# Kernel optimization log

Measured on AMD Instinct MI355X. Metric: run time of the kernel, lower is better.

## Reference

```python
import jax, jax.numpy as jnp
import numpy as np

N_NODES = 16384   # dim_size (number of aggregation groups)
DEG = 16          # neighbors per node
H = 128           # hidden_dim
E = N_NODES * DEG # total neighbor rows


def setup_inputs() -> dict:
    key = jax.random.key(0)
    k1, k2, k3 = jax.random.split(key, 3)
    x = jax.random.normal(k1, (E, H), dtype=jnp.float32)
    # sorted segment ids, DEG neighbors per node (ragged in general; uniform here)
    index = jnp.repeat(jnp.arange(N_NODES, dtype=jnp.int32), DEG)
    # torch LSTM params: gates stacked [i, f, g, o] -> [4H, H]
    W_ih = jax.random.normal(k2, (4 * H, H), dtype=jnp.float32) * 0.02  # xavier gain=0.02 scale
    W_hh = jax.random.normal(k3, (4 * H, H), dtype=jnp.float32) * (1.0 / np.sqrt(H))
    b_ih = jnp.zeros((4 * H,), jnp.float32)
    b_hh = jnp.zeros((4 * H,), jnp.float32)
    return {"x": x, "index": index, "W_ih": W_ih, "W_hh": W_hh,
            "b_ih": b_ih, "b_hh": b_hh, "dim_size": N_NODES}


def reference(x, index, W_ih, W_hh, b_ih, b_hh, dim_size):
    # Faithful to LSTMAggregator.forward: per-group gather of neighbor rows,
    # single-layer LSTM over each group's sequence, final hidden state h_n
    # written to out[group]; empty groups stay zero. (The original's randperm
    # shuffle is nondeterministic and omitted: neighbors kept in index order.)
    x = jnp.nan_to_num(x, nan=0.0)
    E_, Hd = x.shape

    # --- pack ragged groups into a padded [N, L, H] tensor ---
    order = jnp.argsort(index, stable=True)
    idx_s = index[order]
    counts = jax.ops.segment_sum(jnp.ones((E_,), jnp.int32), idx_s, num_segments=dim_size)
    starts = jnp.cumsum(counts) - counts           # exclusive prefix sum
    pos = jnp.arange(E_, dtype=jnp.int32) - starts[idx_s]  # position within group
    L = int(jnp.max(counts))                       # static at call time (concrete inputs)

    x_s = x[order]
    padded = jnp.zeros((dim_size, L, Hd), x.dtype).at[idx_s, pos].set(x_s)  # [N, L, H]
    valid = jnp.arange(L)[None, :] < counts[:, None]                        # [N, L]

    # --- batched masked LSTM scan over time ---
    bias = b_ih + b_hh
    h0 = jnp.zeros((dim_size, Hd), x.dtype)

    def step(carry, inp):
        h, c = carry
        xt, m = inp                                 # xt: [N, H], m: [N]
        gates = xt @ W_ih.T + h @ W_hh.T + bias     # [N, 4H], gate order i,f,g,o
        i, f, g, o = jnp.split(gates, 4, axis=-1)
        i = jax.nn.sigmoid(i); f = jax.nn.sigmoid(f)
        g = jnp.tanh(g);       o = jax.nn.sigmoid(o)
        c_new = f * c + i * g
        h_new = o * jnp.tanh(c_new)
        m = m[:, None]
        return (jnp.where(m, h_new, h), jnp.where(m, c_new, c)), None

    xs = (jnp.swapaxes(padded, 0, 1), valid.T)      # time-major [L, N, H], [L, N]
    (h_final, _), _ = jax.lax.scan(step, (h0, h0), xs)
    return jnp.nan_to_num(h_final, nan=0.0)        # [dim_size, H]
```

## Files before the change

### kernel.cpp

```cpp
#include <hip/hip_runtime.h>

#define DEG      16
#define HDIM     128
#define MB       32
#define NTHREADS 512

typedef __attribute__((ext_vector_type(8))) short  short8;
typedef __attribute__((ext_vector_type(4))) float  floatx4;

__device__ __forceinline__ unsigned short f2bf(float f) {
  union { float f; unsigned int u; } v; v.f = f;
  unsigned int u = v.u;
  u += 0x7fffu + ((u >> 16) & 1u);
  return (unsigned short)(u >> 16);
}

__device__ __forceinline__ float fsig(float x) {
  return __builtin_amdgcn_rcpf(1.0f + __expf(-x));
}
__device__ __forceinline__ float ftanh(float x) {
  return 1.0f - 2.0f * __builtin_amdgcn_rcpf(1.0f + __expf(2.0f * x));
}

__global__ void convert_w_kernel(const float* __restrict__ Wih,
                                 const float* __restrict__ Whh,
                                 unsigned short* __restrict__ Wsw) {
  int i    = blockIdx.x * 256 + threadIdx.x;
  int lane = i & 63;
  int frag = i >> 6;
  int kt = frag >> 5;
  int wg = frag & 31;
  int w  = wg >> 2;
  int g  = wg & 3;
  int j  = g * 128 + w * 16 + (lane & 15);
  int k0 = kt * 32 + (lane >> 4) * 8;
  const float* src = (k0 < HDIM) ? (Wih + (size_t)j * HDIM + k0)
                                 : (Whh + (size_t)j * HDIM + (k0 - HDIM));
  short8 o;
  #pragma unroll
  for (int e = 0; e < 8; ++e) o[e] = (short)f2bf(src[e]);
  *(short8*)(Wsw + (size_t)i * 8) = o;
}

__global__ __launch_bounds__(NTHREADS, 2)
void lstm_agg_kernel(const float* __restrict__ x,
                     const float* __restrict__ b_ih,
                     const float* __restrict__ b_hh,
                     const unsigned short* __restrict__ Wsw,
                     float* __restrict__ out) {
  __shared__ __align__(16) unsigned short As[2][MB * 256];

  const int tid  = threadIdx.x;
  const int w_id = tid >> 6;
  const int lane = tid & 63;
  const int l15  = lane & 15;
  const int q    = lane >> 4;
  const int node0 = blockIdx.x * MB;

  const int j_g = w_id * 16 + l15;

  float bias[4];
  #pragma unroll
  for (int g = 0; g < 4; ++g) bias[g] = b_ih[g * 128 + j_g] + b_hh[g * 128 + j_g];

  short8 breg[2][4];
  #pragma unroll
  for (int kt = 0; kt < 2; ++kt)
    #pragma unroll
    for (int g = 0; g < 4; ++g) {
      int fi = kt * 32 + w_id * 4 + g;
      breg[kt][g] = *(const short8*)(Wsw + ((size_t)fi * 64 + lane) * 8);
    }

  floatx4 c[2], h[2];
  #pragma unroll
  for (int mt = 0; mt < 2; ++mt) {
    floatx4 z = {0.0f, 0.0f, 0.0f, 0.0f};
    c[mt] = z; h[mt] = z;
  }

  const int m_x = tid >> 4;
  const int kc  = tid & 15;
  const float* xbase = x + ((size_t)(node0 + m_x) * DEG) * HDIM + kc * 8;
  const int xch = (kc ^ (m_x & 7)) * 8;
  const int hchunk = (HDIM + j_g) >> 3;
  const int hkl = j_g & 7;

  floatx4 xp0 = ((const floatx4*)xbase)[0];
  floatx4 xp1 = ((const floatx4*)xbase)[1];

  {
    short8 p;
    #pragma unroll
    for (int e = 0; e < 4; ++e) { p[e] = (short)f2bf(xp0[e]); p[e + 4] = (short)f2bf(xp1[e]); }
    *(short8*)&As[0][m_x * 256 + xch] = p;
    unsigned short hz = f2bf(0.0f);
    #pragma unroll
    for (int mt = 0; mt < 2; ++mt)
      #pragma unroll
      for (int r = 0; r < 4; ++r) {
        int m = mt * 16 + q * 4 + r;
        As[0][m * 256 + ((hchunk ^ (m & 7)) << 3) + hkl] = hz;
      }
  }
  xp0 = ((const floatx4*)(xbase + HDIM))[0];
  xp1 = ((const floatx4*)(xbase + HDIM))[1];

  #pragma unroll 1
  for (int t = 0; t < DEG; ++t) {
    __syncthreads();
    const int buf = t & 1;

    const unsigned short* Wp = Wsw;
    asm volatile("" : "+s"(Wp));

    floatx4 acc[4][2];
    #pragma unroll
    for (int g = 0; g < 4; ++g) {
      floatx4 bv = {bias[g], bias[g], bias[g], bias[g]};
      #pragma unroll
      for (int mt = 0; mt < 2; ++mt) acc[g][mt] = bv;
    }

    #pragma unroll
    for (int kt = 0; kt < 8; ++kt) {
      short8 af[2];
      #pragma unroll
      for (int mt = 0; mt < 2; ++mt) {
        int m = mt * 16 + l15;
        int chunk = (kt * 4 + q) ^ (m & 7);
        af[mt] = *(const short8*)&As[buf][m * 256 + chunk * 8];
      }
      short8 bfr[4];
      if (kt < 2) {
        #pragma unroll
        for (int g = 0; g < 4; ++g) bfr[g] = breg[kt][g];
      } else {
        #pragma unroll
        for (int g = 0; g < 4; ++g) {
          int fi = kt * 32 + w_id * 4 + g;
          bfr[g] = *(const short8*)(Wp + ((size_t)fi * 64 + lane) * 8);
        }
      }
      #pragma unroll
      for (int g = 0; g < 4; ++g)
        #pragma unroll
        for (int mt = 0; mt < 2; ++mt)
          acc[g][mt] = __builtin_amdgcn_mfma_f32_16x16x32_bf16(af[mt], bfr[g], acc[g][mt], 0, 0, 0);
    }

    #pragma unroll
    for (int mt = 0; mt < 2; ++mt)
      #pragma unroll
      for (int r = 0; r < 4; ++r) {
        float iv = fsig (acc[0][mt][r]);
        float fv = fsig (acc[1][mt][r]);
        float gv = ftanh(acc[2][mt][r]);
        float ov = fsig (acc[3][mt][r]);
        float cn = fv * c[mt][r] + iv * gv;
        c[mt][r] = cn;
        float hv = ov * ftanh(cn);
        h[mt][r] = hv;
        if (t + 1 < DEG) {
          int m = mt * 16 + q * 4 + r;
          As[buf ^ 1][m * 256 + ((hchunk ^ (m & 7)) << 3) + hkl] = f2bf(hv);
        }
      }

    if (t + 1 < DEG) {
      short8 p;
      #pragma unroll
      for (int e = 0; e < 4; ++e) { p[e] = (short)f2bf(xp0[e]); p[e + 4] = (short)f2bf(xp1[e]); }
      *(short8*)&As[buf ^ 1][m_x * 256 + xch] = p;
      if (t + 2 < DEG) {
        const float* xb = xbase + (size_t)(t + 2) * HDIM;
        xp0 = ((const floatx4*)xb)[0];
        xp1 = ((const floatx4*)xb)[1];
      }
    }
  }

  #pragma unroll
  for (int mt = 0; mt < 2; ++mt)
    #pragma unroll
    for (int r = 0; r < 4; ++r) {
      int m = mt * 16 + q * 4 + r;
      out[(size_t)(node0 + m) * HDIM + j_g] = h[mt][r];
    }
}

extern "C" void kernel_launch(void* const* d_in, const int* in_sizes, int n_in,
                              void* d_out, int out_size, void* d_ws, size_t ws_size,
                              hipStream_t stream) {
  const float* x   = (const float*)d_in[0];
  const float* Wih = (const float*)d_in[2];
  const float* Whh = (const float*)d_in[3];
  const float* bih = (const float*)d_in[4];
  const float* bhh = (const float*)d_in[5];
  unsigned short* Wsw = (unsigned short*)d_ws;
  float* out = (float*)d_out;

  hipLaunchKernelGGL(convert_w_kernel, dim3(64), dim3(256), 0, stream, Wih, Whh, Wsw);

  int nodes   = in_sizes[0] / (DEG * HDIM);
  int nblocks = nodes / MB;
  hipLaunchKernelGGL(lstm_agg_kernel, dim3(nblocks), dim3(NTHREADS), 0, stream,
                     x, bih, bhh, Wsw, out);
}
```

Before: 280.8 us.

## Software-pipeline input projection ahead of recurrence; split X/H LDS and stage weights

The LSTM step now computes the input projection x_{t+1}·W_ih one step early, interleaved with the activation of step t, so each step's critical path only carries the h·W_hh MFMAs. X and H get separate double-buffered LDS arrays with a new swizzle. Part of W_ih is staged in LDS while the rest stays in registers or global memory. bf16 packing now uses v_cvt_pk_bf16_f32, and the time loop is unrolled by two with ping-pong accumulators. The cost is more accumulator registers and about 32KB of extra LDS, which may reduce occupancy below the 2-block launch bound.

Result: faster. 262.0 us (-6.7%).

```diff
diff --git a/kernel.cpp b/kernel.cpp
--- a/kernel.cpp
+++ b/kernel.cpp
@@ -7,12 +7,21 @@
 
 typedef __attribute__((ext_vector_type(8))) short  short8;
 typedef __attribute__((ext_vector_type(4))) float  floatx4;
+typedef __attribute__((ext_vector_type(4))) unsigned int uintx4;
+
+#define MFMA(A,B,C) __builtin_amdgcn_mfma_f32_16x16x32_bf16(A,B,C,0,0,0)
 
 __device__ __forceinline__ unsigned short f2bf(float f) {
   union { float f; unsigned int u; } v; v.f = f;
   unsigned int u = v.u;
   u += 0x7fffu + ((u >> 16) & 1u);
   return (unsigned short)(u >> 16);
+}
+
+__device__ __forceinline__ unsigned int cvtpk(float lo, float hi) {
+  unsigned int r;
+  asm("v_cvt_pk_bf16_f32 %0, %1, %2" : "=v"(r) : "v"(lo), "v"(hi));
+  return r;
 }
 
 __device__ __forceinline__ float fsig(float x) {
@@ -42,13 +51,100 @@
   *(short8*)(Wsw + (size_t)i * 8) = o;
 }
 
+#define ACT_X(MT, PAR, ACCP, ACCQ, LAST_, CS)                                  \
+  {                                                                            \
+    float hv[4];                                                               \
+    _Pragma("unroll")                                                          \
+    for (int r = 0; r < 4; ++r) {                                              \
+      float iv = fsig (ACCP[0][MT][r]);                                        \
+      float fv = fsig (ACCP[1][MT][r]);                                        \
+      float gv = ftanh(ACCP[2][MT][r]);                                        \
+      float ov = fsig (ACCP[3][MT][r]);                                        \
+      float cn = fv * CS[r] + iv * gv;                                         \
+      CS[r] = cn;                                                              \
+      hv[r] = ov * ftanh(cn);                                                  \
+    }                                                                          \
+    if (LAST_) {                                                               \
+      float* ob = out + (size_t)(node0 + MT * 16 + q * 4) * HDIM + j_g;        \
+      _Pragma("unroll")                                                        \
+      for (int r = 0; r < 4; ++r) ob[r * HDIM] = hv[r];                        \
+    } else {                                                                   \
+      unsigned int p01 = cvtpk(hv[0], hv[1]);                                  \
+      unsigned int p23 = cvtpk(hv[2], hv[3]);                                  \
+      *(unsigned short*)(hwp[0] + ((PAR ^ 1) * 8192 + MT * 4096)) = (unsigned short)p01;         \
+      *(unsigned short*)(hwp[1] + ((PAR ^ 1) * 8192 + MT * 4096)) = (unsigned short)(p01 >> 16); \
+      *(unsigned short*)(hwp[2] + ((PAR ^ 1) * 8192 + MT * 4096)) = (unsigned short)p23;         \
+      *(unsigned short*)(hwp[3] + ((PAR ^ 1) * 8192 + MT * 4096)) = (unsigned short)(p23 >> 16); \
+            \
+      short8 ax0 = *(const short8*)(xsE + (PAR ^ 1) * 8192 + MT * 4096 + 0);   \
+      short8 ax1 = *(const short8*)(xsO + (PAR ^ 1) * 8192 + MT * 4096 + 64);  \
+      short8 ax2 = *(const short8*)(xsE + (PAR ^ 1) * 8192 + MT * 4096 + 128); \
+      short8 ax3 = *(const short8*)(xsO + (PAR ^ 1) * 8192 + MT * 4096 + 192); \
+      short8 w2[4];                                                            \
+      _Pragma("unroll")                                                        \
+      for (int g = 0; g < 4; ++g) w2[g] = *(const short8*)(wlB + g * 1024);    \
+      _Pragma("unroll")                                                        \
+      for (int g = 0; g < 4; ++g) {                                            \
+        floatx4 bv = {bias[g], bias[g], bias[g], bias[g]};                     \
+        floatx4 t0 = MFMA(ax0, breg[0][g], bv);                                \
+        t0 = MFMA(ax1, breg[1][g], t0);                                        \
+        t0 = MFMA(ax2, w2[g], t0);                                             \
+        ACCQ[g][MT] = MFMA(ax3, b3[g], t0);                                    \
+      }                                                                        \
+    }                                                                          \
+  }
+
+#define STEP(T, PAR, ACCP, ACCQ, WITH_H, LAST_)                                \
+  {                                                                            \
+    const unsigned short* Wp = Wsw;                                            \
+    asm volatile("" : "+s"(Wp));                     \
+    if (WITH_H) {                                                              \
+      _Pragma("unroll")                                                        \
+      for (int kh = 0; kh < 4; ++kh) {                                         \
+        const unsigned short* Wk = Wp + ((size_t)((4 + kh) * 32 + w_id * 4) * 64 + lane) * 8; \
+        short8 bfr[4];                                                         \
+        _Pragma("unroll")                                                      \
+        for (int g = 0; g < 4; ++g) bfr[g] = *(const short8*)(Wk + g * 512);   \
+        const char* hb = (kh & 1) ? hsO : hsE;                                 \
+        short8 ah0 = *(const short8*)(hb + PAR * 8192 + 0    + kh * 64);       \
+        short8 ah1 = *(const short8*)(hb + PAR * 8192 + 4096 + kh * 64);       \
+        _Pragma("unroll")                                                      \
+        for (int g = 0; g < 4; ++g) {                                          \
+          ACCP[g][0] = MFMA(ah0, bfr[g], ACCP[g][0]);                          \
+          ACCP[g][1] = MFMA(ah1, bfr[g], ACCP[g][1]);                          \
+        }                                                                      \
+      }                                                                        \
+    }                                                                          \
+    short8 b3[4];                                                              \
+    if (!LAST_) {                                                              \
+      const unsigned short* W3 = Wp + ((size_t)(96 + w_id * 4) * 64 + lane) * 8; \
+      _Pragma("unroll")                                                        \
+      for (int g = 0; g < 4; ++g) b3[g] = *(const short8*)(W3 + g * 512);      \
+    }                                                                          \
+    ACT_X(0, PAR, ACCP, ACCQ, LAST_, cs0)                                      \
+    ACT_X(1, PAR, ACCP, ACCQ, LAST_, cs1)                                      \
+    if (!LAST_ && (T) + 2 < DEG) {                                             \
+      uintx4 p;                                                                \
+      p[0] = cvtpk(xp0[0], xp0[1]); p[1] = cvtpk(xp0[2], xp0[3]);              \
+      p[2] = cvtpk(xp1[0], xp1[1]); p[3] = cvtpk(xp1[2], xp1[3]);              \
+      *(uintx4*)(xsW + PAR * 8192) = p;                                        \
+      if ((T) + 3 < DEG) {                                                     \
+        const float* xq_ = xb0 + (size_t)((T) + 3) * HDIM;                     \
+        xp0 = ((const floatx4*)xq_)[0]; xp1 = ((const floatx4*)xq_)[1];        \
+      }                                                                        \
+    }                                                                          \
+    __syncthreads();                                                           \
+  }
+
 __global__ __launch_bounds__(NTHREADS, 2)
 void lstm_agg_kernel(const float* __restrict__ x,
                      const float* __restrict__ b_ih,
                      const float* __restrict__ b_hh,
                      const unsigned short* __restrict__ Wsw,
                      float* __restrict__ out) {
-  __shared__ __align__(16) unsigned short As[2][MB * 256];
+  __shared__ __align__(16) unsigned short Xs[2 * MB * HDIM];
+  __shared__ __align__(16) unsigned short Hs[2 * MB * HDIM];
+  __shared__ __align__(16) unsigned short Wl[32 * 512];
 
   const int tid  = threadIdx.x;
   const int w_id = tid >> 6;
@@ -56,7 +152,6 @@
   const int l15  = lane & 15;
   const int q    = lane >> 4;
   const int node0 = blockIdx.x * MB;
-
   const int j_g = w_id * 16 + l15;
 
   float bias[4];
@@ -72,121 +167,91 @@
       breg[kt][g] = *(const short8*)(Wsw + ((size_t)fi * 64 + lane) * 8);
     }
 
-  floatx4 c[2], h[2];
-  #pragma unroll
-  for (int mt = 0; mt < 2; ++mt) {
-    floatx4 z = {0.0f, 0.0f, 0.0f, 0.0f};
-    c[mt] = z; h[mt] = z;
+  #pragma unroll
+  for (int i = 0; i < 4; ++i) {
+    int o = tid * 32 + i * 8;
+    *(short8*)&Wl[o] = *(const short8*)(Wsw + 2 * 32 * 512 + o);
+  }
+
+  const int fA  = (l15 & 7) ^ ((l15 & 8) >> 2);
+  const int qx  = (q ^ (fA & 3)) << 4;
+  const int f64 = (fA >> 2) << 6;
+  const char* xsE = (const char*)Xs + l15 * 256 + qx + f64;
+  const char* xsO = (const char*)Xs + l15 * 256 + qx - f64;
+  const char* hsE = (const char*)Hs + l15 * 256 + qx + f64;
+  const char* hsO = (const char*)Hs + l15 * 256 + qx - f64;
+
+  const char* wlB = (const char*)Wl + w_id * 4096 + lane * 16;
+
+  const int hc  = j_g >> 3;
+  const int hkl = j_g & 7;
+  char* hwp[4];
+  #pragma unroll
+  for (int r = 0; r < 4; ++r) {
+    int m  = q * 4 + r;
+    int fr = (m & 7) ^ ((m & 8) >> 2);
+    hwp[r] = (char*)Hs + m * 256 + ((hc ^ fr) << 4) + hkl * 2;
   }
 
   const int m_x = tid >> 4;
   const int kc  = tid & 15;
-  const float* xbase = x + ((size_t)(node0 + m_x) * DEG) * HDIM + kc * 8;
-  const int xch = (kc ^ (m_x & 7)) * 8;
-  const int hchunk = (HDIM + j_g) >> 3;
-  const int hkl = j_g & 7;
-
-  floatx4 xp0 = ((const floatx4*)xbase)[0];
-  floatx4 xp1 = ((const floatx4*)xbase)[1];
+  const int fX  = (m_x & 7) ^ ((m_x & 8) >> 2);
+  const float* xb0 = x + ((size_t)(node0 + m_x) * DEG) * HDIM + kc * 8;
+  char* xsW = (char*)Xs + m_x * 256 + ((kc ^ fX) << 4);
+
+  floatx4 cs0 = {0.f, 0.f, 0.f, 0.f};
+  floatx4 cs1 = {0.f, 0.f, 0.f, 0.f};
+  floatx4 accA[4][2], accB[4][2];
+  floatx4 xp0, xp1;
 
   {
-    short8 p;
+    floatx4 u0 = ((const floatx4*)xb0)[0], u1 = ((const floatx4*)xb0)[1];
+    uintx4 p;
+    p[0] = cvtpk(u0[0], u0[1]); p[1] = cvtpk(u0[2], u0[3]);
+    p[2] = cvtpk(u1[0], u1[1]); p[3] = cvtpk(u1[2], u1[3]);
+    *(uintx4*)xsW = p;
+    u0 = ((const floatx4*)(xb0 + HDIM))[0]; u1 = ((const floatx4*)(xb0 + HDIM))[1];
+    p[0] = cvtpk(u0[0], u0[1]); p[1] = cvtpk(u0[2], u0[3]);
+    p[2] = cvtpk(u1[0], u1[1]); p[3] = cvtpk(u1[2], u1[3]);
+    *(uintx4*)(xsW + 8192) = p;
+    xp0 = ((const floatx4*)(xb0 + 2 * HDIM))[0];
+    xp1 = ((const floatx4*)(xb0 + 2 * HDIM))[1];
+  }
+  __syncthreads();
+
+  {
+    short8 b3p[4];
+    const unsigned short* W3 = Wsw + ((size_t)(96 + w_id * 4) * 64 + lane) * 8;
     #pragma unroll
-    for (int e = 0; e < 4; ++e) { p[e] = (short)f2bf(xp0[e]); p[e + 4] = (short)f2bf(xp1[e]); }
-    *(short8*)&As[0][m_x * 256 + xch] = p;
-    unsigned short hz = f2bf(0.0f);
+    for (int g = 0; g < 4; ++g) b3p[g] = *(const short8*)(W3 + g * 512);
     #pragma unroll
-    for (int mt = 0; mt < 2; ++mt)
+    for (int mt = 0; mt < 2; ++mt) {
+      short8 ax0 = *(const short8*)(xsE + mt * 4096 + 0);
+      short8 ax1 = *(const short8*)(xsO + mt * 4096 + 64);
+      short8 ax2 = *(const short8*)(xsE + mt * 4096 + 128);
+      short8 ax3 = *(const short8*)(xsO + mt * 4096 + 192);
+      short8 w2[4];
       #pragma unroll
-      for (int r = 0; r < 4; ++r) {
-        int m = mt * 16 + q * 4 + r;
-        As[0][m * 256 + ((hchunk ^ (m & 7)) << 3) + hkl] = hz;
-      }
-  }
-  xp0 = ((const floatx4*)(xbase + HDIM))[0];
-  xp1 = ((const floatx4*)(xbase + HDIM))[1];
-
-  #pragma unroll 1
-  for (int t = 0; t < DEG; ++t) {
-    __syncthreads();
-    const int buf = t & 1;
-
-    const unsigned short* Wp = Wsw;
-    asm volatile("" : "+s"(Wp));
-
-    floatx4 acc[4][2];
-    #pragma unroll
-    for (int g = 0; g < 4; ++g) {
-      floatx4 bv = {bias[g], bias[g], bias[g], bias[g]};
+      for (int g = 0; g < 4; ++g) w2[g] = *(const short8*)(wlB + g * 1024);
       #pragma unroll
-      for (int mt = 0; mt < 2; ++mt) acc[g][mt] = bv;
-    }
-
-    #pragma unroll
-    for (int kt = 0; kt < 8; ++kt) {
-      short8 af[2];
-      #pragma unroll
-      for (int mt = 0; mt < 2; ++mt) {
-        int m = mt * 16 + l15;
-        int chunk = (kt * 4 + q) ^ (m & 7);
-        af[mt] = *(const short8*)&As[buf][m * 256 + chunk * 8];
-      }
-      short8 bfr[4];
-      if (kt < 2) {
-        #pragma unroll
-        for (int g = 0; g < 4; ++g) bfr[g] = breg[kt][g];
-      } else {
-        #pragma unroll
-        for (int g = 0; g < 4; ++g) {
-          int fi = kt * 32 + w_id * 4 + g;
-          bfr[g] = *(const short8*)(Wp + ((size_t)fi * 64 + lane) * 8);
-        }
-      }
-      #pragma unroll
-      for (int g = 0; g < 4; ++g)
-        #pragma unroll
-        for (int mt = 0; mt < 2; ++mt)
-          acc[g][mt] = __builtin_amdgcn_mfma_f32_16x16x32_bf16(af[mt], bfr[g], acc[g][mt], 0, 0, 0);
-    }
-
-    #pragma unroll
-    for (int mt = 0; mt < 2; ++mt)
-      #pragma unroll
-      for (int r = 0; r < 4; ++r) {
-        float iv = fsig (acc[0][mt][r]);
-        float fv = fsig (acc[1][mt][r]);
-        float gv = ftanh(acc[2][mt][r]);
-        float ov = fsig (acc[3][mt][r]);
-        float cn = fv * c[mt][r] + iv * gv;
-        c[mt][r] = cn;
-        float hv = ov * ftanh(cn);
-        h[mt][r] = hv;
-        if (t + 1 < DEG) {
-          int m = mt * 16 + q * 4 + r;
-          As[buf ^ 1][m * 256 + ((hchunk ^ (m & 7)) << 3) + hkl] = f2bf(hv);
-        }
-      }
-
-    if (t + 1 < DEG) {
-      short8 p;
-      #pragma unroll
-      for (int e = 0; e < 4; ++e) { p[e] = (short)f2bf(xp0[e]); p[e + 4] = (short)f2bf(xp1[e]); }
-      *(short8*)&As[buf ^ 1][m_x * 256 + xch] = p;
-      if (t + 2 < DEG) {
-        const float* xb = xbase + (size_t)(t + 2) * HDIM;
-        xp0 = ((const floatx4*)xb)[0];
-        xp1 = ((const floatx4*)xb)[1];
+      for (int g = 0; g < 4; ++g) {
+        floatx4 bv = {bias[g], bias[g], bias[g], bias[g]};
+        floatx4 t0 = MFMA(ax0, breg[0][g], bv);
+        t0 = MFMA(ax1, breg[1][g], t0);
+        t0 = MFMA(ax2, w2[g], t0);
+        accA[g][mt] = MFMA(ax3, b3p[g], t0);
       }
     }
   }
-
-  #pragma unroll
-  for (int mt = 0; mt < 2; ++mt)
-    #pragma unroll
-    for (int r = 0; r < 4; ++r) {
-      int m = mt * 16 + q * 4 + r;
-      out[(size_t)(node0 + m) * HDIM + j_g] = h[mt][r];
-    }
+  __syncthreads();
+
+  STEP(0, 0, accA, accB, 0, 0)
+  #pragma unroll 1
+  for (int t = 1; t < 15; t += 2) {
+    STEP(t,     1, accB, accA, 1, 0)
+    STEP(t + 1, 0, accA, accB, 1, 0)
+  }
+  STEP(15, 1, accB, accA, 1, 1)
 }
 
 extern "C" void kernel_launch(void* const* d_in, const int* in_sizes, int n_in,
```
